# Kernel optimization log

Hardware: AMD Instinct MI355X
Metric: run time of the kernel (lower is better)

## Reference

```python
import jax, jax.numpy as jnp
import numpy as np

DIM = 1024
NUM_HEADS = 16
HEAD_DIM = DIM // NUM_HEADS
SCALE = HEAD_DIM ** -0.5


def setup_inputs() -> dict:
    key = jax.random.key(0)
    k1, k2, k3, k4 = jax.random.split(key, 4)
    B, N = 2, 2048
    x = jax.random.normal(k1, (B, N, DIM), dtype=jnp.float32)
    # qkv: Linear(dim, 3*dim, bias=False); torch stores weight as [out, in]
    W_qkv = jax.random.normal(k2, (3 * DIM, DIM), dtype=jnp.float32) * (DIM ** -0.5)
    # proj: Linear(dim, dim, bias=True)
    W_proj = jax.random.normal(k3, (DIM, DIM), dtype=jnp.float32) * (DIM ** -0.5)
    b_proj = jax.random.normal(k4, (DIM,), dtype=jnp.float32) * 0.01
    return {"x": x, "W_qkv": W_qkv, "W_proj": W_proj, "b_proj": b_proj}


def reference(x, W_qkv, W_proj, b_proj):
    B, N, C = x.shape
    H, D = NUM_HEADS, HEAD_DIM
    # qkv projection: [B,N,3C] -> [3,B,H,N,D]
    qkv = jnp.einsum('bnc,oc->bno', x, W_qkv)
    qkv = qkv.reshape(B, N, 3, H, D).transpose(2, 0, 3, 1, 4)
    q, k, v = qkv[0] * SCALE, qkv[1], qkv[2]
    # full attention matrix [B,H,N,N] (faithful to manual impl)
    attn = jnp.einsum('bhqd,bhkd->bhqk', q, k)
    attn = jax.nn.softmax(attn, axis=-1)
    # dropout p=0.0 -> identity (eval semantics)
    out = jnp.einsum('bhqk,bhkd->bhqd', attn, v)  # [B,H,N,D]
    out = out.transpose(0, 2, 1, 3).reshape(B, N, C)
    out = jnp.einsum('bnc,oc->bno', out, W_proj) + b_proj
    return out
```

## Files before the change

kernel.cpp:

```cpp
#include <hip/hip_runtime.h>
#include <math.h>

#define BATCH 2
#define NTOK  2048
#define DIMC  1024
#define NH    16
#define HD    64
#define SOFT_K2 0.18033688011112042f

typedef __bf16 bf16;
typedef __attribute__((ext_vector_type(8))) __bf16 bf16x8;
typedef __attribute__((ext_vector_type(4))) __bf16 bf16x4;
typedef __attribute__((ext_vector_type(4))) float f32x4;

__device__ __forceinline__ void load_lds16(const void* g, void* l) {
    __builtin_amdgcn_global_load_lds(
        (const __attribute__((address_space(1))) void*)g,
        (__attribute__((address_space(3))) void*)l, 16, 0, 0);
}
__device__ __forceinline__ f32x4 mfma16(bf16x8 a, bf16x8 b, f32x4 c) {
    return __builtin_amdgcn_mfma_f32_16x16x32_bf16(a, b, c, 0, 0, 0);
}

__global__ __launch_bounds__(256) void cast3(
    const float* __restrict__ x,  const float* __restrict__ w1, const float* __restrict__ w2,
    bf16* __restrict__ xb, bf16* __restrict__ w1b, bf16* __restrict__ w2b)
{
    int blk = blockIdx.x;
    const float* src; bf16* dst; size_t base;
    if (blk < 4096)      { src = x;  dst = xb;  base = (size_t)blk * 1024; }
    else if (blk < 7168) { src = w1; dst = w1b; base = (size_t)(blk - 4096) * 1024; }
    else                 { src = w2; dst = w2b; base = (size_t)(blk - 7168) * 1024; }
    size_t i = base + (size_t)threadIdx.x * 4;
    float4 v = *(const float4*)(src + i);
    bf16x4 r;
    r[0] = (bf16)v.x; r[1] = (bf16)v.y; r[2] = (bf16)v.z; r[3] = (bf16)v.w;
    *(bf16x4*)(dst + i) = r;
}

__global__ __launch_bounds__(256) void gemm_qkv(
    const bf16* __restrict__ A, const bf16* __restrict__ B,
    bf16* __restrict__ Cq, bf16* __restrict__ vt,
    int M, int N, int K)
{
    __shared__ __align__(16) bf16 As[128 * 32];
    __shared__ __align__(16) bf16 Bs[128 * 32];

    const int tid  = threadIdx.x;
    const int w    = tid >> 6, lane = tid & 63;
    const int wm   = w & 1,  wn = w >> 1;
    const int m0   = blockIdx.y * 128, n0 = blockIdx.x * 128;
    const int lm   = lane & 15, quad = lane >> 4;

    const bf16* Ag[2]; const bf16* Bg[2];
#pragma unroll
    for (int t = 0; t < 2; ++t) {
        int c = t * 256 + tid;
        Ag[t] = A + (size_t)(m0 + (c & 127)) * K + (c >> 7) * 8;
        Bg[t] = B + (size_t)(n0 + (c & 127)) * K + (c >> 7) * 8;
    }

    f32x4 acc[4][4];
    f32x4 z4 = {0.f, 0.f, 0.f, 0.f};
#pragma unroll
    for (int i = 0; i < 4; ++i)
#pragma unroll
        for (int j = 0; j < 4; ++j) acc[i][j] = z4;

    for (int kt = 0; kt < K; kt += 32) {
        __syncthreads();
#pragma unroll
        for (int t = 0; t < 2; ++t) {
            load_lds16(Ag[t] + kt, As + (t * 256 + w * 64) * 8);
            load_lds16(Bg[t] + kt, Bs + (t * 256 + w * 64) * 8);
        }
        __syncthreads();

        bf16x8 af[4], bf_[4];
#pragma unroll
        for (int mi = 0; mi < 4; ++mi)
            af[mi] = *(const bf16x8*)(As + (quad * 128 + wm * 64 + mi * 16 + lm) * 8);
#pragma unroll
        for (int ni = 0; ni < 4; ++ni)
            bf_[ni] = *(const bf16x8*)(Bs + (quad * 128 + wn * 64 + ni * 16 + lm) * 8);
#pragma unroll
        for (int mi = 0; mi < 4; ++mi)
#pragma unroll
            for (int ni = 0; ni < 4; ++ni)
                acc[mi][ni] = mfma16(af[mi], bf_[ni], acc[mi][ni]);
    }

    if (n0 >= 2048) {
#pragma unroll
        for (int ni = 0; ni < 4; ++ni) {
            const int c  = n0 + wn * 64 + ni * 16 + lm - 2048;
            const int hh = c >> 6, dd = c & 63;
#pragma unroll
            for (int mi = 0; mi < 4; ++mi) {
                const int rowb = m0 + wm * 64 + mi * 16 + quad * 4;
                const int bb = rowb >> 11, tok = rowb & 2047;
                bf16x4 pk;
                pk[0] = (bf16)acc[mi][ni][0]; pk[1] = (bf16)acc[mi][ni][1];
                pk[2] = (bf16)acc[mi][ni][2]; pk[3] = (bf16)acc[mi][ni][3];
                *(bf16x4*)(vt + ((size_t)((bb * NH + hh) * HD + dd)) * NTOK + tok) = pk;
            }
        }
    } else {
#pragma unroll
        for (int ni = 0; ni < 4; ++ni) {
            const int col = n0 + wn * 64 + ni * 16 + lm;
#pragma unroll
            for (int mi = 0; mi < 4; ++mi)
#pragma unroll
                for (int r = 0; r < 4; ++r) {
                    const int row = m0 + wm * 64 + mi * 16 + quad * 4 + r;
                    Cq[(size_t)row * N + col] = (bf16)acc[mi][ni][r];
                }
        }
    }
}

__global__ __launch_bounds__(256) void gemm_proj(
    const bf16* __restrict__ A, const bf16* __restrict__ B,
    const float* __restrict__ bias, float* __restrict__ C,
    int M, int N, int K)
{
    __shared__ __align__(16) bf16 As[64 * 32];
    __shared__ __align__(16) bf16 Bs[128 * 32];

    const int tid  = threadIdx.x;
    const int w    = tid >> 6, lane = tid & 63;
    const int wm   = w & 1,  wn = w >> 1;
    const int m0   = blockIdx.y * 64, n0 = blockIdx.x * 128;
    const int lm   = lane & 15, quad = lane >> 4;

    const bf16* Ag; const bf16* Bg[2];
    {
        int c = tid;
        Ag = A + (size_t)(m0 + (c & 63)) * K + (c >> 6) * 8;
    }
#pragma unroll
    for (int t = 0; t < 2; ++t) {
        int c = t * 256 + tid;
        Bg[t] = B + (size_t)(n0 + (c & 127)) * K + (c >> 7) * 8;
    }

    f32x4 acc[2][4];
    f32x4 z4 = {0.f, 0.f, 0.f, 0.f};
#pragma unroll
    for (int i = 0; i < 2; ++i)
#pragma unroll
        for (int j = 0; j < 4; ++j) acc[i][j] = z4;

    for (int kt = 0; kt < K; kt += 32) {
        __syncthreads();
        load_lds16(Ag + kt, As + (w * 64) * 8);
#pragma unroll
        for (int t = 0; t < 2; ++t)
            load_lds16(Bg[t] + kt, Bs + (t * 256 + w * 64) * 8);
        __syncthreads();

        bf16x8 af[2], bf_[4];
#pragma unroll
        for (int mi = 0; mi < 2; ++mi)
            af[mi] = *(const bf16x8*)(As + (quad * 64 + wm * 32 + mi * 16 + lm) * 8);
#pragma unroll
        for (int ni = 0; ni < 4; ++ni)
            bf_[ni] = *(const bf16x8*)(Bs + (quad * 128 + wn * 64 + ni * 16 + lm) * 8);
#pragma unroll
        for (int mi = 0; mi < 2; ++mi)
#pragma unroll
            for (int ni = 0; ni < 4; ++ni)
                acc[mi][ni] = mfma16(af[mi], bf_[ni], acc[mi][ni]);
    }

#pragma unroll
    for (int ni = 0; ni < 4; ++ni) {
        const int col = n0 + wn * 64 + ni * 16 + lm;
        const float bi = bias[col];
#pragma unroll
        for (int mi = 0; mi < 2; ++mi)
#pragma unroll
            for (int r = 0; r < 4; ++r) {
                const int row = m0 + wm * 32 + mi * 16 + quad * 4 + r;
                C[(size_t)row * N + col] = acc[mi][ni][r] + bi;
            }
    }
}

__global__ __launch_bounds__(256, 2) void attn_mfma(
    const bf16* __restrict__ qkv,
    const bf16* __restrict__ Vt,
    bf16* __restrict__ att)
{
    __shared__ __align__(16) bf16 Ks[2][64 * 64];
    __shared__ __align__(16) bf16 Vs[2][64 * 64];
    __shared__ __align__(16) bf16 Ps[2][128 * 72];

    const int n0 = blockIdx.x * 128, h = blockIdx.y, b = blockIdx.z;
    const int tid = threadIdx.x, w = tid >> 6, lane = tid & 63;
    const int lm = lane & 15, quad = lane >> 4;

    const size_t rs = (size_t)(3 * DIMC);
    const bf16* qbase  = qkv + (size_t)b * NTOK * rs + h * HD;
    const bf16* kbase  = qbase + DIMC;
    const bf16* vtbase = Vt + ((size_t)(b * NH + h) * HD) * NTOK;

    bf16x8 aq[2][2];
#pragma unroll
    for (int g = 0; g < 2; ++g)
#pragma unroll
        for (int s2 = 0; s2 < 2; ++s2)
            aq[g][s2] = *(const bf16x8*)(qbase
                + (size_t)(n0 + w * 32 + g * 16 + lm) * rs + s2 * 32 + quad * 8);

    const int l0 = (w * 2 + 0) * 64 + lane, l1 = (w * 2 + 1) * 64 + lane;
    const bf16* kg0 = kbase + (size_t)(l0 & 63) * rs + (l0 >> 6) * 8;
    const bf16* kg1 = kbase + (size_t)(l1 & 63) * rs + (l1 >> 6) * 8;
    const bf16* vg0 = vtbase + (size_t)(l0 & 63) * NTOK + (l0 >> 6) * 8;
    const bf16* vg1 = vtbase + (size_t)(l1 & 63) * NTOK + (l1 >> 6) * 8;

#define STAGE_K(tile, dst) do { \
    load_lds16(kg0 + (size_t)(tile) * 64 * rs, (dst) + (w * 2 + 0) * 512); \
    load_lds16(kg1 + (size_t)(tile) * 64 * rs, (dst) + (w * 2 + 1) * 512); } while (0)
#define STAGE_V(tile, dst) do { \
    load_lds16(vg0 + (size_t)(tile) * 64, (dst) + (w * 2 + 0) * 512); \
    load_lds16(vg1 + (size_t)(tile) * 64, (dst) + (w * 2 + 1) * 512); } while (0)

    f32x4 O[2][4];
    f32x4 z4 = {0.f, 0.f, 0.f, 0.f};
#pragma unroll
    for (int g = 0; g < 2; ++g)
#pragma unroll
        for (int ni = 0; ni < 4; ++ni) O[g][ni] = z4;
    float lsum[2][4] = {{0.f, 0.f, 0.f, 0.f}, {0.f, 0.f, 0.f, 0.f}};

#define COMPUTE_S_PS(Ksb, Psb) do {                                           \
    f32x4 S[2][4];                                                            \
    for (int g = 0; g < 2; ++g)                                               \
        for (int ni = 0; ni < 4; ++ni) S[g][ni] = z4;                         \
    for (int s2 = 0; s2 < 2; ++s2)                                            \
        for (int ni = 0; ni < 4; ++ni) {                                      \
            bf16x8 bk = *(const bf16x8*)((Ksb)                                \
                + ((s2 * 4 + quad) * 64 + ni * 16 + lm) * 8);                 \
            S[0][ni] = mfma16(aq[0][s2], bk, S[0][ni]);                       \
            S[1][ni] = mfma16(aq[1][s2], bk, S[1][ni]);                       \
        }                                                                     \
    for (int g = 0; g < 2; ++g)                                               \
        for (int ni = 0; ni < 4; ++ni)                                        \
            for (int r = 0; r < 4; ++r) {                                     \
                const float p = __builtin_amdgcn_exp2f(S[g][ni][r] * SOFT_K2);\
                (Psb)[(w * 32 + g * 16 + quad * 4 + r) * 72 + ni * 16 + lm]   \
                    = (bf16)p;                                                \
                lsum[g][r] += p;                                              \
            }                                                                 \
} while (0)

#define COMPUTE_PV(Psb, Vsb) do {                                             \
    for (int s2 = 0; s2 < 2; ++s2) {                                          \
        bf16x8 ap0 = *(const bf16x8*)((Psb)                                   \
            + (w * 32 + lm) * 72 + s2 * 32 + quad * 8);                       \
        bf16x8 ap1 = *(const bf16x8*)((Psb)                                   \
            + (w * 32 + 16 + lm) * 72 + s2 * 32 + quad * 8);                  \
        for (int ni = 0; ni < 4; ++ni) {                                      \
            bf16x8 bv = *(const bf16x8*)((Vsb)                                \
                + ((s2 * 4 + quad) * 64 + ni * 16 + lm) * 8);                 \
            O[0][ni] = mfma16(ap0, bv, O[0][ni]);                             \
            O[1][ni] = mfma16(ap1, bv, O[1][ni]);                             \
        }                                                                     \
    }                                                                         \
} while (0)

    const int NT = NTOK / 64;

    STAGE_K(0, Ks[0]);
    STAGE_V(0, Vs[0]);
    STAGE_K(1, Ks[1]);
    __syncthreads();
    COMPUTE_S_PS(Ks[0], Ps[0]);

    for (int t = 0; t < NT; ++t) {
        __syncthreads();
        if (t + 2 < NT) STAGE_K(t + 2, Ks[t & 1]);
        if (t + 1 < NT) STAGE_V(t + 1, Vs[(t + 1) & 1]);
        if (t + 1 < NT) COMPUTE_S_PS(Ks[(t + 1) & 1], Ps[(t + 1) & 1]);
        COMPUTE_PV(Ps[t & 1], Vs[t & 1]);
    }

#undef STAGE_K
#undef STAGE_V
#undef COMPUTE_S_PS
#undef COMPUTE_PV

#pragma unroll
    for (int g = 0; g < 2; ++g)
#pragma unroll
        for (int r = 0; r < 4; ++r) {
#pragma unroll
            for (int msk = 1; msk < 16; msk <<= 1)
                lsum[g][r] += __shfl_xor(lsum[g][r], msk);
        }

#pragma unroll
    for (int g = 0; g < 2; ++g)
#pragma unroll
        for (int r = 0; r < 4; ++r) {
            const float invl = 1.0f / lsum[g][r];
            const size_t row = (size_t)(b * NTOK + n0 + w * 32 + g * 16 + quad * 4 + r);
#pragma unroll
            for (int ni = 0; ni < 4; ++ni)
                att[row * DIMC + h * HD + ni * 16 + lm] = (bf16)(O[g][ni][r] * invl);
        }
}

extern "C" void kernel_launch(void* const* d_in, const int* in_sizes, int n_in,
                              void* d_out, int out_size, void* d_ws, size_t ws_size,
                              hipStream_t stream)
{
    const float* x      = (const float*)d_in[0];
    const float* W_qkv  = (const float*)d_in[1];
    const float* W_proj = (const float*)d_in[2];
    const float* b_proj = (const float*)d_in[3];
    float* out = (float*)d_out;

    char* ws = (char*)d_ws;
    bf16* xb   = (bf16*)ws;
    bf16* w1b  = (bf16*)(ws + (8u  << 20));
    bf16* w2b  = (bf16*)(ws + (14u << 20));
    bf16* qkvb = (bf16*)(ws + (16u << 20));
    bf16* vt   = (bf16*)(ws + (40u << 20));
    bf16* attb = (bf16*)(ws + (48u << 20));

    const int M = BATCH * NTOK;

    cast3<<<8192, 256, 0, stream>>>(x, W_qkv, W_proj, xb, w1b, w2b);

    gemm_qkv<<<dim3((3 * DIMC) / 128, M / 128), 256, 0, stream>>>(
        xb, w1b, qkvb, vt, M, 3 * DIMC, DIMC);

    attn_mfma<<<dim3(NTOK / 128, NH, BATCH), 256, 0, stream>>>(qkvb, vt, attb);

    gemm_proj<<<dim3(DIMC / 128, M / 64), 256, 0, stream>>>(
        attb, w2b, b_proj, out, M, DIMC, DIMC);
}
```

Measured before the change: 232.8 us.

## Double-buffer LDS in QKV and proj GEMMs and stage V-transpose stores through LDS

Measured after the change: 239.1 us. +2.7%, slower.

```diff
diff --git a/kernel.cpp b/kernel.cpp
--- a/kernel.cpp
+++ b/kernel.cpp
@@ -43,8 +43,7 @@
     bf16* __restrict__ Cq, bf16* __restrict__ vt,
     int M, int N, int K)
 {
-    __shared__ __align__(16) bf16 As[128 * 32];
-    __shared__ __align__(16) bf16 Bs[128 * 32];
+    __shared__ __align__(16) bf16 smem[17408];
 
     const int tid  = threadIdx.x;
     const int w    = tid >> 6, lane = tid & 63;
@@ -67,43 +66,57 @@
 #pragma unroll
         for (int j = 0; j < 4; ++j) acc[i][j] = z4;
 
-    for (int kt = 0; kt < K; kt += 32) {
-        __syncthreads();
-#pragma unroll
-        for (int t = 0; t < 2; ++t) {
-            load_lds16(Ag[t] + kt, As + (t * 256 + w * 64) * 8);
-            load_lds16(Bg[t] + kt, Bs + (t * 256 + w * 64) * 8);
-        }
-        __syncthreads();
-
+#define QKV_STAGE(kt, b_) do {                                                  \
+    for (int t = 0; t < 2; ++t) {                                               \
+        load_lds16(Ag[t] + (kt), smem + (b_) * 4096 + (t * 256 + w * 64) * 8);  \
+        load_lds16(Bg[t] + (kt), smem + 8192 + (b_) * 4096 + (t * 256 + w * 64) * 8); \
+    } } while (0)
+
+    const int NI = K / 32;
+    QKV_STAGE(0, 0);
+    __syncthreads();
+    for (int it = 0; it < NI; ++it) {
+        const int buf = it & 1;
+        if (it + 1 < NI) QKV_STAGE((it + 1) * 32, buf ^ 1);
+        const bf16* Asb = smem + buf * 4096;
+        const bf16* Bsb = smem + 8192 + buf * 4096;
         bf16x8 af[4], bf_[4];
 #pragma unroll
         for (int mi = 0; mi < 4; ++mi)
-            af[mi] = *(const bf16x8*)(As + (quad * 128 + wm * 64 + mi * 16 + lm) * 8);
+            af[mi] = *(const bf16x8*)(Asb + (quad * 128 + wm * 64 + mi * 16 + lm) * 8);
 #pragma unroll
         for (int ni = 0; ni < 4; ++ni)
-            bf_[ni] = *(const bf16x8*)(Bs + (quad * 128 + wn * 64 + ni * 16 + lm) * 8);
+            bf_[ni] = *(const bf16x8*)(Bsb + (quad * 128 + wn * 64 + ni * 16 + lm) * 8);
 #pragma unroll
         for (int mi = 0; mi < 4; ++mi)
 #pragma unroll
             for (int ni = 0; ni < 4; ++ni)
                 acc[mi][ni] = mfma16(af[mi], bf_[ni], acc[mi][ni]);
-    }
+        __syncthreads();
+    }
+#undef QKV_STAGE
 
     if (n0 >= 2048) {
+        bf16* T = smem;
 #pragma unroll
         for (int ni = 0; ni < 4; ++ni) {
-            const int c  = n0 + wn * 64 + ni * 16 + lm - 2048;
-            const int hh = c >> 6, dd = c & 63;
-#pragma unroll
-            for (int mi = 0; mi < 4; ++mi) {
-                const int rowb = m0 + wm * 64 + mi * 16 + quad * 4;
-                const int bb = rowb >> 11, tok = rowb & 2047;
-                bf16x4 pk;
-                pk[0] = (bf16)acc[mi][ni][0]; pk[1] = (bf16)acc[mi][ni][1];
-                pk[2] = (bf16)acc[mi][ni][2]; pk[3] = (bf16)acc[mi][ni][3];
-                *(bf16x4*)(vt + ((size_t)((bb * NH + hh) * HD + dd)) * NTOK + tok) = pk;
-            }
+            const int dl = wn * 64 + ni * 16 + lm;
+#pragma unroll
+            for (int mi = 0; mi < 4; ++mi)
+#pragma unroll
+                for (int r = 0; r < 4; ++r)
+                    T[dl * 136 + wm * 64 + mi * 16 + quad * 4 + r] = (bf16)acc[mi][ni][r];
+        }
+        __syncthreads();
+        const int gcol0 = n0 - 2048;
+        const int bb = m0 >> 11, tokbase = m0 & 2047;
+#pragma unroll
+        for (int rep = 0; rep < 8; ++rep) {
+            const int g = rep * 256 + tid;
+            const int d = g >> 4, tc = g & 15;
+            bf16x8 v = *(const bf16x8*)&T[d * 136 + tc * 8];
+            const int gcol = gcol0 + d, hh = gcol >> 6, dd = gcol & 63;
+            *(bf16x8*)(vt + ((size_t)((bb * NH + hh) * HD + dd)) * NTOK + tokbase + tc * 8) = v;
         }
     } else {
 #pragma unroll
@@ -125,8 +138,7 @@
     const float* __restrict__ bias, float* __restrict__ C,
     int M, int N, int K)
 {
-    __shared__ __align__(16) bf16 As[64 * 32];
-    __shared__ __align__(16) bf16 Bs[128 * 32];
+    __shared__ __align__(16) bf16 smem[12288];
 
     const int tid  = threadIdx.x;
     const int w    = tid >> 6, lane = tid & 63;
@@ -134,11 +146,8 @@
     const int m0   = blockIdx.y * 64, n0 = blockIdx.x * 128;
     const int lm   = lane & 15, quad = lane >> 4;
 
-    const bf16* Ag; const bf16* Bg[2];
-    {
-        int c = tid;
-        Ag = A + (size_t)(m0 + (c & 63)) * K + (c >> 6) * 8;
-    }
+    const bf16* Ag = A + (size_t)(m0 + (tid & 63)) * K + (tid >> 6) * 8;
+    const bf16* Bg[2];
 #pragma unroll
     for (int t = 0; t < 2; ++t) {
         int c = t * 256 + tid;
@@ -152,27 +161,35 @@
 #pragma unroll
         for (int j = 0; j < 4; ++j) acc[i][j] = z4;
 
-    for (int kt = 0; kt < K; kt += 32) {
-        __syncthreads();
-        load_lds16(Ag + kt, As + (w * 64) * 8);
-#pragma unroll
-        for (int t = 0; t < 2; ++t)
-            load_lds16(Bg[t] + kt, Bs + (t * 256 + w * 64) * 8);
-        __syncthreads();
-
+#define PROJ_STAGE(kt, b_) do {                                                 \
+    load_lds16(Ag + (kt), smem + (b_) * 2048 + (w * 64) * 8);                   \
+    for (int t = 0; t < 2; ++t)                                                 \
+        load_lds16(Bg[t] + (kt), smem + 4096 + (b_) * 4096 + (t * 256 + w * 64) * 8); \
+    } while (0)
+
+    const int NI = K / 32;
+    PROJ_STAGE(0, 0);
+    __syncthreads();
+    for (int it = 0; it < NI; ++it) {
+        const int buf = it & 1;
+        if (it + 1 < NI) PROJ_STAGE((it + 1) * 32, buf ^ 1);
+        const bf16* Asb = smem + buf * 2048;
+        const bf16* Bsb = smem + 4096 + buf * 4096;
         bf16x8 af[2], bf_[4];
 #pragma unroll
         for (int mi = 0; mi < 2; ++mi)
-            af[mi] = *(const bf16x8*)(As + (quad * 64 + wm * 32 + mi * 16 + lm) * 8);
+            af[mi] = *(const bf16x8*)(Asb + (quad * 64 + wm * 32 + mi * 16 + lm) * 8);
 #pragma unroll
         for (int ni = 0; ni < 4; ++ni)
-            bf_[ni] = *(const bf16x8*)(Bs + (quad * 128 + wn * 64 + ni * 16 + lm) * 8);
+            bf_[ni] = *(const bf16x8*)(Bsb + (quad * 128 + wn * 64 + ni * 16 + lm) * 8);
 #pragma unroll
         for (int mi = 0; mi < 2; ++mi)
 #pragma unroll
             for (int ni = 0; ni < 4; ++ni)
                 acc[mi][ni] = mfma16(af[mi], bf_[ni], acc[mi][ni]);
-    }
+        __syncthreads();
+    }
+#undef PROJ_STAGE
 
 #pragma unroll
     for (int ni = 0; ni < 4; ++ni) {
```

## Replace LDS-staged GEMMs with single-wave register-direct 64x64 tiles

Applied to the files above, without the earlier changes.

After: 263.8 us. 13.3% more time.

```diff
diff --git a/kernel.cpp b/kernel.cpp
--- a/kernel.cpp
+++ b/kernel.cpp
@@ -38,27 +38,41 @@
     *(bf16x4*)(dst + i) = r;
 }
 
-__global__ __launch_bounds__(256) void gemm_qkv(
+__device__ __forceinline__ void gemm_tile_64x64(
+    const bf16* __restrict__ A, const bf16* __restrict__ B,
+    int m0, int n0, int K, int lm, int quad, f32x4 acc[4][4])
+{
+    const bf16* Ab[4]; const bf16* Bb[4];
+#pragma unroll
+    for (int i = 0; i < 4; ++i) {
+        Ab[i] = A + (size_t)(m0 + i * 16 + lm) * K + quad * 8;
+        Bb[i] = B + (size_t)(n0 + i * 16 + lm) * K + quad * 8;
+    }
+#pragma unroll
+    for (int kk = 0; kk < 1024; kk += 32) {
+        bf16x8 af[4], bf_[4];
+#pragma unroll
+        for (int i = 0; i < 4; ++i) af[i]  = *(const bf16x8*)(Ab[i] + kk);
+#pragma unroll
+        for (int i = 0; i < 4; ++i) bf_[i] = *(const bf16x8*)(Bb[i] + kk);
+#pragma unroll
+        for (int mi = 0; mi < 4; ++mi)
+#pragma unroll
+            for (int ni = 0; ni < 4; ++ni)
+                acc[mi][ni] = mfma16(af[mi], bf_[ni], acc[mi][ni]);
+    }
+}
+
+__global__ __launch_bounds__(64, 3) void gemm_qkv(
     const bf16* __restrict__ A, const bf16* __restrict__ B,
     bf16* __restrict__ Cq, bf16* __restrict__ vt,
     int M, int N, int K)
 {
-    __shared__ __align__(16) bf16 As[128 * 32];
-    __shared__ __align__(16) bf16 Bs[128 * 32];
-
-    const int tid  = threadIdx.x;
-    const int w    = tid >> 6, lane = tid & 63;
-    const int wm   = w & 1,  wn = w >> 1;
-    const int m0   = blockIdx.y * 128, n0 = blockIdx.x * 128;
-    const int lm   = lane & 15, quad = lane >> 4;
-
-    const bf16* Ag[2]; const bf16* Bg[2];
-#pragma unroll
-    for (int t = 0; t < 2; ++t) {
-        int c = t * 256 + tid;
-        Ag[t] = A + (size_t)(m0 + (c & 127)) * K + (c >> 7) * 8;
-        Bg[t] = B + (size_t)(n0 + (c & 127)) * K + (c >> 7) * 8;
-    }
+    __shared__ __align__(16) bf16 T[64 * 72];
+
+    const int lane = threadIdx.x;
+    const int lm = lane & 15, quad = lane >> 4;
+    const int m0 = blockIdx.y * 64, n0 = blockIdx.x * 64;
 
     f32x4 acc[4][4];
     f32x4 z4 = {0.f, 0.f, 0.f, 0.f};
@@ -67,122 +81,70 @@
 #pragma unroll
         for (int j = 0; j < 4; ++j) acc[i][j] = z4;
 
-    for (int kt = 0; kt < K; kt += 32) {
-        __syncthreads();
-#pragma unroll
-        for (int t = 0; t < 2; ++t) {
-            load_lds16(Ag[t] + kt, As + (t * 256 + w * 64) * 8);
-            load_lds16(Bg[t] + kt, Bs + (t * 256 + w * 64) * 8);
-        }
-        __syncthreads();
-
-        bf16x8 af[4], bf_[4];
-#pragma unroll
-        for (int mi = 0; mi < 4; ++mi)
-            af[mi] = *(const bf16x8*)(As + (quad * 128 + wm * 64 + mi * 16 + lm) * 8);
-#pragma unroll
-        for (int ni = 0; ni < 4; ++ni)
-            bf_[ni] = *(const bf16x8*)(Bs + (quad * 128 + wn * 64 + ni * 16 + lm) * 8);
-#pragma unroll
-        for (int mi = 0; mi < 4; ++mi)
-#pragma unroll
-            for (int ni = 0; ni < 4; ++ni)
-                acc[mi][ni] = mfma16(af[mi], bf_[ni], acc[mi][ni]);
-    }
+    gemm_tile_64x64(A, B, m0, n0, K, lm, quad, acc);
 
     if (n0 >= 2048) {
 #pragma unroll
         for (int ni = 0; ni < 4; ++ni) {
-            const int c  = n0 + wn * 64 + ni * 16 + lm - 2048;
-            const int hh = c >> 6, dd = c & 63;
-#pragma unroll
-            for (int mi = 0; mi < 4; ++mi) {
-                const int rowb = m0 + wm * 64 + mi * 16 + quad * 4;
-                const int bb = rowb >> 11, tok = rowb & 2047;
-                bf16x4 pk;
-                pk[0] = (bf16)acc[mi][ni][0]; pk[1] = (bf16)acc[mi][ni][1];
-                pk[2] = (bf16)acc[mi][ni][2]; pk[3] = (bf16)acc[mi][ni][3];
-                *(bf16x4*)(vt + ((size_t)((bb * NH + hh) * HD + dd)) * NTOK + tok) = pk;
-            }
+            const int dl = ni * 16 + lm;
+#pragma unroll
+            for (int mi = 0; mi < 4; ++mi)
+#pragma unroll
+                for (int r = 0; r < 4; ++r)
+                    T[dl * 72 + mi * 16 + quad * 4 + r] = (bf16)acc[mi][ni][r];
+        }
+        const int gcol0 = n0 - 2048;
+        const int bb = m0 >> 11, tokbase = m0 & 2047;
+#pragma unroll
+        for (int rep = 0; rep < 8; ++rep) {
+            const int g = rep * 64 + lane;
+            const int d = g >> 3, tc = g & 7;
+            bf16x8 v = *(const bf16x8*)&T[d * 72 + tc * 8];
+            const int gcol = gcol0 + d, hh = gcol >> 6, dd = gcol & 63;
+            *(bf16x8*)(vt + ((size_t)((bb * NH + hh) * HD + dd)) * NTOK + tokbase + tc * 8) = v;
         }
     } else {
 #pragma unroll
         for (int ni = 0; ni < 4; ++ni) {
-            const int col = n0 + wn * 64 + ni * 16 + lm;
+            const int col = n0 + ni * 16 + lm;
 #pragma unroll
             for (int mi = 0; mi < 4; ++mi)
 #pragma unroll
                 for (int r = 0; r < 4; ++r) {
-                    const int row = m0 + wm * 64 + mi * 16 + quad * 4 + r;
+                    const int row = m0 + mi * 16 + quad * 4 + r;
                     Cq[(size_t)row * N + col] = (bf16)acc[mi][ni][r];
                 }
         }
     }
 }
 
-__global__ __launch_bounds__(256) void gemm_proj(
+__global__ __launch_bounds__(64, 3) void gemm_proj(
     const bf16* __restrict__ A, const bf16* __restrict__ B,
     const float* __restrict__ bias, float* __restrict__ C,
     int M, int N, int K)
 {
-    __shared__ __align__(16) bf16 As[64 * 32];
-    __shared__ __align__(16) bf16 Bs[128 * 32];
-
-    const int tid  = threadIdx.x;
-    const int w    = tid >> 6, lane = tid & 63;
-    const int wm   = w & 1,  wn = w >> 1;
-    const int m0   = blockIdx.y * 64, n0 = blockIdx.x * 128;
-    const int lm   = lane & 15, quad = lane >> 4;
-
-    const bf16* Ag; const bf16* Bg[2];
-    {
-        int c = tid;
-        Ag = A + (size_t)(m0 + (c & 63)) * K + (c >> 6) * 8;
-    }
-#pragma unroll
-    for (int t = 0; t < 2; ++t) {
-        int c = t * 256 + tid;
-        Bg[t] = B + (size_t)(n0 + (c & 127)) * K + (c >> 7) * 8;
-    }
-
-    f32x4 acc[2][4];
+    const int lane = threadIdx.x;
+    const int lm = lane & 15, quad = lane >> 4;
+    const int m0 = blockIdx.y * 64, n0 = blockIdx.x * 64;
+
+    f32x4 acc[4][4];
     f32x4 z4 = {0.f, 0.f, 0.f, 0.f};
 #pragma unroll
-    for (int i = 0; i < 2; ++i)
+    for (int i = 0; i < 4; ++i)
 #pragma unroll
         for (int j = 0; j < 4; ++j) acc[i][j] = z4;
 
-    for (int kt = 0; kt < K; kt += 32) {
-        __syncthreads();
-        load_lds16(Ag + kt, As + (w * 64) * 8);
-#pragma unroll
-        for (int t = 0; t < 2; ++t)
-            load_lds16(Bg[t] + kt, Bs + (t * 256 + w * 64) * 8);
-        __syncthreads();
-
-        bf16x8 af[2], bf_[4];
-#pragma unroll
-        for (int mi = 0; mi < 2; ++mi)
-            af[mi] = *(const bf16x8*)(As + (quad * 64 + wm * 32 + mi * 16 + lm) * 8);
-#pragma unroll
-        for (int ni = 0; ni < 4; ++ni)
-            bf_[ni] = *(const bf16x8*)(Bs + (quad * 128 + wn * 64 + ni * 16 + lm) * 8);
-#pragma unroll
-        for (int mi = 0; mi < 2; ++mi)
-#pragma unroll
-            for (int ni = 0; ni < 4; ++ni)
-                acc[mi][ni] = mfma16(af[mi], bf_[ni], acc[mi][ni]);
-    }
+    gemm_tile_64x64(A, B, m0, n0, K, lm, quad, acc);
 
 #pragma unroll
     for (int ni = 0; ni < 4; ++ni) {
-        const int col = n0 + wn * 64 + ni * 16 + lm;
+        const int col = n0 + ni * 16 + lm;
         const float bi = bias[col];
 #pragma unroll
-        for (int mi = 0; mi < 2; ++mi)
+        for (int mi = 0; mi < 4; ++mi)
 #pragma unroll
             for (int r = 0; r < 4; ++r) {
-                const int row = m0 + wm * 32 + mi * 16 + quad * 4 + r;
+                const int row = m0 + mi * 16 + quad * 4 + r;
                 C[(size_t)row * N + col] = acc[mi][ni][r] + bi;
             }
     }
@@ -335,11 +297,11 @@
 
     cast3<<<8192, 256, 0, stream>>>(x, W_qkv, W_proj, xb, w1b, w2b);
 
-    gemm_qkv<<<dim3((3 * DIMC) / 128, M / 128), 256, 0, stream>>>(
+    gemm_qkv<<<dim3((3 * DIMC) / 64, M / 64), 64, 0, stream>>>(
         xb, w1b, qkvb, vt, M, 3 * DIMC, DIMC);
 
     attn_mfma<<<dim3(NTOK / 128, NH, BATCH), 256, 0, stream>>>(qkvb, vt, attb);
 
-    gemm_proj<<<dim3(DIMC / 128, M / 64), 256, 0, stream>>>(
+    gemm_proj<<<dim3(DIMC / 64, M / 64), 64, 0, stream>>>(
         attb, w2b, b_proj, out, M, DIMC, DIMC);
 }
```
